# Performance work log

Measured on AMD Instinct MI355X. Metric: run time of the kernel, lower is better.

The kernel has to match this reference:

```python
import jax, jax.numpy as jnp
import numpy as np

B, C, H, W = 16, 512, 64, 64
SCALE = 8
CQK = C // SCALE  # 64
EPS = 1e-6


def setup_inputs() -> dict:
    key = jax.random.key(0)
    ks = jax.random.split(key, 8)
    x = jax.random.normal(ks[0], (B, C, H, W), dtype=jnp.float32)
    # 1x1 conv weights stored as [out_ch, in_ch] (kernel_size=1)
    Wq = jax.random.normal(ks[1], (CQK, C), dtype=jnp.float32) * 0.02
    bq = jnp.zeros((CQK,), dtype=jnp.float32)
    Wk = jax.random.normal(ks[2], (CQK, C), dtype=jnp.float32) * 0.02
    bk = jnp.zeros((CQK,), dtype=jnp.float32)
    Wv = jax.random.normal(ks[3], (C, C), dtype=jnp.float32) * 0.02
    bv = jnp.zeros((C,), dtype=jnp.float32)
    # gamma is initialized to 0 in the module; use a nonzero value so the
    # output is non-trivial for kernel correctness checks.
    gamma = jax.random.normal(ks[4], (1,), dtype=jnp.float32)
    return {"x": x, "Wq": Wq, "bq": bq, "Wk": Wk, "bk": bk,
            "Wv": Wv, "bv": bv, "gamma": gamma}


def _l2norm_ch(t):
    # normalize over the channel axis (dim=-2), matching torch.norm(p=2, dim=-2)
    nrm = jnp.sqrt(jnp.sum(t * t, axis=-2, keepdims=True))
    return t / jnp.maximum(nrm, EPS)


def reference(x, Wq, bq, Wk, bk, Wv, bv, gamma):
    b, c, h, w = x.shape
    n = h * w
    xf = x.reshape(b, c, n)                                   # [B,C,N]
    # 1x1 convs == channel matmuls
    Q = jnp.einsum('oc,bcn->bon', Wq, xf) + bq[None, :, None]  # [B,cqk,N]
    K = jnp.einsum('oc,bcn->bon', Wk, xf) + bk[None, :, None]  # [B,cqk,N]
    V = jnp.einsum('oc,bcn->bon', Wv, xf) + bv[None, :, None]  # [B,C,N]
    Qn = _l2norm_ch(Q).transpose(0, 2, 1)                      # [B,N,cqk]
    Kn = _l2norm_ch(K)                                         # [B,cqk,N]
    # Taylor-softmax surrogate denominator
    denom = n + jnp.einsum('bnc,bc->bn', Qn, Kn.sum(axis=-1))  # [B,N]
    tailor = 1.0 / jnp.maximum(denom, 1e-6)                    # [B,N]
    # KtV accumulation: [B,cqk,C]
    matrix = jnp.einsum('bmn,bcn->bmc', Kn, V)
    value_sum = jnp.sum(V, axis=-1)[:, :, None]                # [B,C,1] -> broadcast
    matrix_sum = value_sum + jnp.einsum('bnm,bmc->bcn', Qn, matrix)  # [B,C,N]
    weight_value = matrix_sum * tailor[:, None, :]             # [B,C,N]
    out = gamma * weight_value.reshape(b, c, h, w)
    return jnp.nan_to_num(out, nan=0.0, posinf=1.0, neginf=-1.0)
```

## Files before the change

### kernel.cpp

```cpp
#include <hip/hip_runtime.h>


typedef __attribute__((ext_vector_type(8))) short short8_t;
typedef __attribute__((ext_vector_type(4))) float f32x4;

__device__ __forceinline__ unsigned short f2bf(float f) {
  union { float f; unsigned u; } v; v.f = f;
  unsigned r = v.u + 0x7FFFu + ((v.u >> 16) & 1u);
  return (unsigned short)(r >> 16);
}
__device__ __forceinline__ float bf2f(unsigned short h) {
  union { unsigned u; float f; } v; v.u = ((unsigned)h) << 16;
  return v.f;
}

#define MFMA(a, b, c) __builtin_amdgcn_mfma_f32_16x16x32_bf16((a), (b), (c), 0, 0, 0)

__global__ void k_prep(const float* __restrict__ Wq, const float* __restrict__ Wk,
                       unsigned short* __restrict__ Wqk,
                       float* __restrict__ xsum, float* __restrict__ Ksum) {
  int idx = blockIdx.x * 256 + threadIdx.x;
  int o = idx >> 9, c = idx & 511;
  float v = (o < 64) ? Wq[o * 512 + c] : Wk[(o - 64) * 512 + c];
  Wqk[idx] = f2bf(v);
  if (idx < 8192) xsum[idx] = 0.f;
  if (idx < 1024) Ksum[idx] = 0.f;
}

__launch_bounds__(256, 2)
__global__ void k_qk(const float* __restrict__ x, const unsigned short* __restrict__ Wqk,
                     const float* __restrict__ bq, const float* __restrict__ bk,
                     unsigned short* __restrict__ QnT, unsigned short* __restrict__ KnG,
                     float* __restrict__ Ksum) {
  __shared__ __align__(16) unsigned char smem[77312];
  unsigned short* SAb[2] = {(unsigned short*)(smem + 0),
                            (unsigned short*)(smem + 18432)};
  unsigned short* SBb[2] = {(unsigned short*)(smem + 36864),
                            (unsigned short*)(smem + 55296)};
  unsigned short* EQ = (unsigned short*)(smem + 0);
  unsigned short* EK = (unsigned short*)(smem + 18432);
  float* ssq   = (float*)(smem + 73728);
  float* invq  = (float*)(smem + 75776);
  float* invk  = (float*)(smem + 76288);
  float* biasL = (float*)(smem + 76800);

  const int t = threadIdx.x;
  const int lane = t & 63, w = t >> 6;
  const int l15 = lane & 15, quad = lane >> 4;
  const int nt = blockIdx.x, b = blockIdx.y;
  const int n0 = nt * 128;
  const float* xb = x + (size_t)b * 512 * 4096;

  if (t < 128) biasL[t] = (t < 64) ? bq[t] : bk[t - 64];

  f32x4 acc[2][8];
#pragma unroll
  for (int i = 0; i < 2; ++i)
#pragma unroll
    for (int j = 0; j < 8; ++j) acc[i][j] = (f32x4){0.f, 0.f, 0.f, 0.f};

  const int nB = t & 127;
  const int cgB = t >> 7;
  const float* bsrc0 = xb + (size_t)(cgB * 32) * 4096 + n0 + nB;

  short8_t apre[4];
  float bpre[32];

#define QK_LOADA(kc_) do {                                                     \
    const int c0_ = (kc_) * 64;                                                \
    _Pragma("unroll")                                                          \
    for (int p = 0; p < 4; ++p) {                                              \
      int gid = t + p * 256; int o_ = gid >> 3, cg = gid & 7;                  \
      apre[p] = *(const short8_t*)(Wqk + o_ * 512 + c0_ + cg * 8);             \
    } } while (0)

#define QK_LOADB(kc_) do {                                                     \
    const float* s_ = bsrc0 + (size_t)(kc_) * 64 * 4096;                       \
    _Pragma("unroll")                                                          \
    for (int i = 0; i < 32; ++i) bpre[i] = s_[(size_t)i * 4096];               \
    } while (0)

#define QK_STORE(pb) do {                                                      \
    unsigned short* SAp = SAb[pb]; unsigned short* SBp = SBb[pb];              \
    _Pragma("unroll")                                                          \
    for (int p = 0; p < 4; ++p) {                                              \
      int gid = t + p * 256; int o_ = gid >> 3, cg = gid & 7;                  \
      *(short8_t*)(SAp + o_ * 72 + cg * 8) = apre[p];                          \
    }                                                                          \
    _Pragma("unroll")                                                          \
    for (int j = 0; j < 4; ++j) {                                              \
      short8_t v_;                                                             \
      _Pragma("unroll")                                                        \
      for (int e = 0; e < 8; ++e) v_[e] = (short)f2bf(bpre[j * 8 + e]);        \
      *(short8_t*)(SBp + nB * 72 + cgB * 32 + j * 8) = v_;                     \
    } } while (0)

#define QK_MM(pb) do {                                                         \
    const unsigned short* SAp = SAb[pb]; const unsigned short* SBp = SBb[pb];  \
    _Pragma("unroll")                                                          \
    for (int s = 0; s < 2; ++s) {                                              \
      short8_t a0 = *(const short8_t*)(SAp + (w * 32 + l15) * 72 + s * 32 + quad * 8);      \
      short8_t a1 = *(const short8_t*)(SAp + (w * 32 + 16 + l15) * 72 + s * 32 + quad * 8); \
      _Pragma("unroll")                                                        \
      for (int tc = 0; tc < 8; ++tc) {                                         \
        short8_t bf_ = *(const short8_t*)(SBp + (tc * 16 + l15) * 72 + s * 32 + quad * 8);  \
        acc[0][tc] = MFMA(a0, bf_, acc[0][tc]);                                \
        acc[1][tc] = MFMA(a1, bf_, acc[1][tc]);                                \
      } } } while (0)

  QK_LOADA(0); QK_LOADB(0);
#pragma unroll
  for (int kc = 0; kc < 8; ++kc) {
    const int pb = kc & 1;
    QK_STORE(pb);
    if (kc < 7) { QK_LOADA(kc + 1); QK_LOADB(kc + 1); }
    __syncthreads();
    QK_MM(pb);
  }
  __syncthreads();

#pragma unroll
  for (int trl = 0; trl < 2; ++trl)
#pragma unroll
    for (int reg = 0; reg < 4; ++reg) {
      int o = w * 32 + trl * 16 + quad * 4 + reg;
      float bias = biasL[o];
#pragma unroll
      for (int tc = 0; tc < 8; ++tc) acc[trl][tc][reg] += bias;
    }

#pragma unroll
  for (int tc = 0; tc < 8; ++tc) {
    float v = 0.f;
#pragma unroll
    for (int trl = 0; trl < 2; ++trl)
#pragma unroll
      for (int reg = 0; reg < 4; ++reg) {
        float q = acc[trl][tc][reg];
        v += q * q;
      }
    v += __shfl_xor(v, 16);
    v += __shfl_xor(v, 32);
    if (quad == 0) ssq[w * 128 + tc * 16 + l15] = v;
  }
  __syncthreads();
  if (t < 128) {
    float qs = ssq[t] + ssq[128 + t];
    float ks = ssq[256 + t] + ssq[384 + t];
    invq[t] = 1.0f / fmaxf(sqrtf(qs), 1e-6f);
    invk[t] = 1.0f / fmaxf(sqrtf(ks), 1e-6f);
  }
  __syncthreads();

  if (w < 2) {
#pragma unroll
    for (int trl = 0; trl < 2; ++trl)
#pragma unroll
      for (int tc = 0; tc < 8; ++tc) {
        int n = tc * 16 + l15;
        float inv = invq[n];
#pragma unroll
        for (int reg = 0; reg < 4; ++reg) {
          int o = w * 32 + trl * 16 + quad * 4 + reg;
          EQ[n * 72 + o] = f2bf(acc[trl][tc][reg] * inv);
        }
      }
  } else {
#pragma unroll
    for (int trl = 0; trl < 2; ++trl)
#pragma unroll
      for (int reg = 0; reg < 4; ++reg) {
        int m = (w - 2) * 32 + trl * 16 + quad * 4 + reg;
        float p = 0.f;
#pragma unroll
        for (int tc = 0; tc < 8; ++tc) {
          int n = tc * 16 + l15;
          float val = acc[trl][tc][reg] * invk[n];
          EK[m * 136 + n] = f2bf(val);
          p += val;
        }
        p += __shfl_xor(p, 1);
        p += __shfl_xor(p, 2);
        p += __shfl_xor(p, 4);
        p += __shfl_xor(p, 8);
        if (l15 == 0) atomicAdd(Ksum + b * 64 + m, p);
      }
  }
  __syncthreads();

  unsigned short* qdst = QnT + ((size_t)b * 4096 + n0) * 64;
#pragma unroll
  for (int p = 0; p < 4; ++p) {
    int idx = t + p * 256;
    int row = idx >> 3, seg = idx & 7;
    *(short8_t*)(qdst + row * 64 + seg * 8) = *(const short8_t*)(EQ + row * 72 + seg * 8);
  }
  unsigned short* kdst = KnG + (size_t)b * 64 * 4096 + n0;
#pragma unroll
  for (int p = 0; p < 4; ++p) {
    int idx = t + p * 256;
    int row = idx >> 4, seg = idx & 15;
    *(short8_t*)(kdst + (size_t)row * 4096 + seg * 8) =
        *(const short8_t*)(EK + row * 136 + seg * 8);
  }
#undef QK_LOADA
#undef QK_LOADB
#undef QK_STORE
#undef QK_MM
}

__launch_bounds__(256, 2)
__global__ void k_t(const float* __restrict__ x, const unsigned short* __restrict__ KnG,
                    float* __restrict__ Tpart, float* __restrict__ xsum,
                    const unsigned short* __restrict__ QnT,
                    const float* __restrict__ Ksum, float* __restrict__ tailor) {
  __shared__ __align__(16) unsigned char smem[55552];
  unsigned short* SAb[2] = {(unsigned short*)(smem + 0),
                            (unsigned short*)(smem + 9216)};
  unsigned short* SBb[2] = {(unsigned short*)(smem + 18432),
                            (unsigned short*)(smem + 36864)};
  float* Ksl = (float*)(smem + 55296);
  const int t = threadIdx.x;
  const int lane = t & 63, w = t >> 6;
  const int l15 = lane & 15, quad = lane >> 4;
  const int ns = blockIdx.x, ct = blockIdx.y, b = blockIdx.z;
  const int c0 = ct * 128;
  const float* xb = x + (size_t)b * 512 * 4096;
  const unsigned short* Knb = KnG + (size_t)b * 64 * 4096 + ns * 512;

  if (t < 64) Ksl[t] = Ksum[b * 64 + t];

  f32x4 acc[4][2];
#pragma unroll
  for (int i = 0; i < 4; ++i)
#pragma unroll
    for (int j = 0; j < 2; ++j) acc[i][j] = (f32x4){0.f, 0.f, 0.f, 0.f};

  const int row = t >> 1, half = t & 1;
  float xs = 0.f;
  const float* bbase = xb + (size_t)(c0 + row) * 4096 + ns * 512 + half * 32;

  short8_t apre[2];
  f32x4 bpre[8];

#define T_LOADA(ch_) do {                                                      \
    _Pragma("unroll")                                                          \
    for (int p = 0; p < 2; ++p) {                                              \
      int gid = t + p * 256; int m_ = gid >> 3, cg = gid & 7;                  \
      apre[p] = *(const short8_t*)(Knb + (size_t)m_ * 4096 + (ch_) * 64 + cg * 8); \
    } } while (0)

#define T_LOADB(ch_) do {                                                      \
    const float* s_ = bbase + (ch_) * 64;                                      \
    _Pragma("unroll")                                                          \
    for (int q = 0; q < 8; ++q) bpre[q] = *(const f32x4*)(s_ + q * 4);         \
    } while (0)

#define T_STORE(pb) do {                                                       \
    unsigned short* SAp = SAb[pb]; unsigned short* SBp = SBb[pb];              \
    _Pragma("unroll")                                                          \
    for (int p = 0; p < 2; ++p) {                                              \
      int gid = t + p * 256; int m_ = gid >> 3, cg = gid & 7;                  \
      *(short8_t*)(SAp + m_ * 72 + cg * 8) = apre[p];                          \
    }                                                                          \
    _Pragma("unroll")                                                          \
    for (int j = 0; j < 4; ++j) {                                              \
      short8_t v_;                                                             \
      _Pragma("unroll")                                                        \
      for (int e = 0; e < 4; ++e) {                                            \
        float f0 = bpre[j * 2][e], f1 = bpre[j * 2 + 1][e];                    \
        xs += f0 + f1;                                                         \
        v_[e] = (short)f2bf(f0); v_[4 + e] = (short)f2bf(f1);                  \
      }                                                                        \
      *(short8_t*)(SBp + row * 72 + half * 32 + j * 8) = v_;                   \
    } } while (0)

#define T_MM(pb) do {                                                          \
    const unsigned short* SAp = SAb[pb]; const unsigned short* SBp = SBb[pb];  \
    _Pragma("unroll")                                                          \
    for (int s = 0; s < 2; ++s) {                                              \
      short8_t af[4];                                                          \
      _Pragma("unroll")                                                        \
      for (int tm = 0; tm < 4; ++tm)                                           \
        af[tm] = *(const short8_t*)(SAp + (tm * 16 + l15) * 72 + s * 32 + quad * 8); \
      _Pragma("unroll")                                                        \
      for (int tcl = 0; tcl < 2; ++tcl) {                                      \
        short8_t bf_ = *(const short8_t*)(SBp + (w * 32 + tcl * 16 + l15) * 72 + s * 32 + quad * 8); \
        _Pragma("unroll")                                                      \
        for (int tm = 0; tm < 4; ++tm) acc[tm][tcl] = MFMA(af[tm], bf_, acc[tm][tcl]); \
      } } } while (0)

  T_LOADA(0); T_LOADB(0);
#pragma unroll
  for (int ch = 0; ch < 8; ++ch) {
    const int pb = ch & 1;
    T_STORE(pb);
    if (ch < 7) { T_LOADA(ch + 1); T_LOADB(ch + 1); }
    __syncthreads();
    if (ch == 0 && t < 128) {
      int n = ns * 512 + ct * 128 + t;
      const unsigned short* q = QnT + ((size_t)b * 4096 + n) * 64;
      float d = 0.f;
#pragma unroll
      for (int s8 = 0; s8 < 8; ++s8) {
        short8_t qv = *(const short8_t*)(q + s8 * 8);
#pragma unroll
        for (int e = 0; e < 8; ++e)
          d += bf2f((unsigned short)qv[e]) * Ksl[s8 * 8 + e];
      }
      tailor[b * 4096 + n] = 1.0f / fmaxf(4096.0f + d, 1e-6f);
    }
    T_MM(pb);
  }

  xs += __shfl_xor(xs, 1);
  if (half == 0) atomicAdd(xsum + b * 512 + c0 + row, xs);
  float* Tp = Tpart + ((size_t)(ns * 16 + b) * 64) * 512;
#pragma unroll
  for (int tm = 0; tm < 4; ++tm)
#pragma unroll
    for (int tcl = 0; tcl < 2; ++tcl)
#pragma unroll
      for (int reg = 0; reg < 4; ++reg) {
        int m = tm * 16 + quad * 4 + reg;
        int c = c0 + w * 32 + tcl * 16 + l15;
        Tp[(size_t)m * 512 + c] = acc[tm][tcl][reg];
      }
#undef T_LOADA
#undef T_LOADB
#undef T_STORE
#undef T_MM
}

__launch_bounds__(256, 2)
__global__ void k_mat(const float* __restrict__ Tpart, const float* __restrict__ Wv,
                      const float* __restrict__ bv, const float* __restrict__ xsum,
                      const float* __restrict__ Ksum,
                      unsigned short* __restrict__ matT, float* __restrict__ Vsum) {
  __shared__ __align__(16) unsigned char smem[27136];
  float* ST = (float*)smem;
  float* SW = (float*)(smem + 17408);
  float* SV = (float*)(smem + 26112);
  const int t = threadIdx.x;
  const int cb = blockIdx.x, b = blockIdx.y;
  const int c0 = cb * 32;
  const int mp = t >> 3, cs = t & 7;
  f32x4 acc0 = (f32x4){0.f, 0.f, 0.f, 0.f};
  f32x4 acc1 = (f32x4){0.f, 0.f, 0.f, 0.f};

  for (int kc = 0; kc < 8; ++kc) {
    __syncthreads();
#pragma unroll
    for (int p = 0; p < 4; ++p) {
      int idx = t + p * 256;
      int row = idx >> 4, f4 = idx & 15;
      const float* tp = Tpart + ((size_t)b * 64 + row) * 512 + kc * 64 + f4 * 4;
      f32x4 s = *(const f32x4*)tp;
#pragma unroll
      for (int ns2 = 1; ns2 < 8; ++ns2)
        s += *(const f32x4*)(tp + (size_t)ns2 * 524288);
      *(f32x4*)(ST + row * 68 + f4 * 4) = s;
    }
#pragma unroll
    for (int p = 0; p < 2; ++p) {
      int idx = t + p * 256;
      int row = idx >> 4, f4 = idx & 15;
      *(f32x4*)(SW + row * 68 + f4 * 4) =
          *(const f32x4*)(Wv + (size_t)(c0 + row) * 512 + kc * 64 + f4 * 4);
    }
    __syncthreads();
#pragma unroll 4
    for (int kk = 0; kk < 64; kk += 4) {
      f32x4 t0 = *(const f32x4*)(ST + (2 * mp) * 68 + kk);
      f32x4 t1 = *(const f32x4*)(ST + (2 * mp + 1) * 68 + kk);
#pragma unroll
      for (int j = 0; j < 4; ++j) {
        f32x4 wv = *(const f32x4*)(SW + (cs + j * 8) * 68 + kk);
#pragma unroll
        for (int e = 0; e < 4; ++e) {
          acc0[j] = fmaf(t0[e], wv[e], acc0[j]);
          acc1[j] = fmaf(t1[e], wv[e], acc1[j]);
        }
      }
    }
  }
  float ks0 = Ksum[b * 64 + 2 * mp];
  float ks1 = Ksum[b * 64 + 2 * mp + 1];
#pragma unroll
  for (int j = 0; j < 4; ++j) {
    int c = c0 + cs + j * 8;
    float bvc = bv[c];
    unsigned lo = f2bf(acc0[j] + bvc * ks0);
    unsigned hi = f2bf(acc1[j] + bvc * ks1);
    *(unsigned*)(matT + ((size_t)b * 512 + c) * 64 + 2 * mp) = lo | (hi << 16);
  }
  {
    int cc = t >> 3, kp = t & 7;
    const float* wr = Wv + (size_t)(c0 + cc) * 512 + kp * 64;
    const float* xr = xsum + b * 512 + kp * 64;
    float s = 0.f;
    for (int i = 0; i < 64; ++i) s += wr[i] * xr[i];
    SV[cc * 8 + kp] = s;
  }
  __syncthreads();
  if (t < 32) {
    float s = 0.f;
#pragma unroll
    for (int i = 0; i < 8; ++i) s += SV[t * 8 + i];
    int c = c0 + t;
    Vsum[b * 512 + c] = s + 4096.0f * bv[c];
  }
}

__launch_bounds__(256, 2)
__global__ void k_out(const unsigned short* __restrict__ QnT,
                      const unsigned short* __restrict__ matT,
                      const float* __restrict__ tailG, const float* __restrict__ Vsum,
                      const float* __restrict__ gamma, float* __restrict__ out) {
  __shared__ __align__(16) unsigned char smem[37888];
  unsigned short* SA = (unsigned short*)smem;
  unsigned short* SB = (unsigned short*)(smem + 18432);
  float* tail = (float*)(smem + 36864);
  float* vs   = (float*)(smem + 37376);
  const int t = threadIdx.x;
  const int lane = t & 63, w = t >> 6;
  const int l15 = lane & 15, quad = lane >> 4;
  const int nt = blockIdx.x, ct = blockIdx.y, b = blockIdx.z;
  const int n0 = nt * 128, c0 = ct * 128;

  const unsigned short* asrc = matT + ((size_t)b * 512 + c0) * 64;
  const unsigned short* bsrc = QnT + ((size_t)b * 4096 + n0) * 64;
#pragma unroll
  for (int p = 0; p < 4; ++p) {
    int idx = t + p * 256;
    int row = idx >> 3, seg = idx & 7;
    *(short8_t*)(SA + row * 72 + seg * 8) = *(const short8_t*)(asrc + row * 64 + seg * 8);
    *(short8_t*)(SB + row * 72 + seg * 8) = *(const short8_t*)(bsrc + row * 64 + seg * 8);
  }
  if (t < 128) tail[t] = tailG[b * 4096 + n0 + t];
  else if (t < 256) vs[t - 128] = Vsum[b * 512 + c0 + (t - 128)];
  __syncthreads();

  f32x4 acc[2][8];
#pragma unroll
  for (int i = 0; i < 2; ++i)
#pragma unroll
    for (int j = 0; j < 8; ++j) acc[i][j] = (f32x4){0.f, 0.f, 0.f, 0.f};

#pragma unroll
  for (int s = 0; s < 2; ++s) {
    short8_t a0 = *(const short8_t*)(SA + (w * 32 + l15) * 72 + s * 32 + quad * 8);
    short8_t a1 = *(const short8_t*)(SA + (w * 32 + 16 + l15) * 72 + s * 32 + quad * 8);
#pragma unroll
    for (int tc = 0; tc < 8; ++tc) {
      short8_t bfr = *(const short8_t*)(SB + (tc * 16 + l15) * 72 + s * 32 + quad * 8);
      acc[0][tc] = MFMA(a0, bfr, acc[0][tc]);
      acc[1][tc] = MFMA(a1, bfr, acc[1][tc]);
    }
  }
  const float g = gamma[0];
  float* ob = out + (size_t)b * 512 * 4096;
#pragma unroll
  for (int trl = 0; trl < 2; ++trl)
#pragma unroll
    for (int tc = 0; tc < 8; ++tc) {
      int n = tc * 16 + l15;
      float tl = tail[n] * g;
#pragma unroll
      for (int reg = 0; reg < 4; ++reg) {
        int cl = w * 32 + trl * 16 + quad * 4 + reg;
        float val = tl * (vs[cl] + acc[trl][tc][reg]);
        ob[(size_t)(c0 + cl) * 4096 + n0 + n] = val;
      }
    }
}

extern "C" void kernel_launch(void* const* d_in, const int* in_sizes, int n_in,
                              void* d_out, int out_size, void* d_ws, size_t ws_size,
                              hipStream_t stream) {
  const float* x     = (const float*)d_in[0];
  const float* Wq    = (const float*)d_in[1];
  const float* bq    = (const float*)d_in[2];
  const float* Wk    = (const float*)d_in[3];
  const float* bk    = (const float*)d_in[4];
  const float* Wv    = (const float*)d_in[5];
  const float* bv    = (const float*)d_in[6];
  const float* gamma = (const float*)d_in[7];
  float* out = (float*)d_out;
  char* ws = (char*)d_ws;

  float* Tpart  = (float*)(ws + 0);
  float* xsum   = (float*)(ws + 16777216);
  float* Ksum   = (float*)(ws + 16809984);
  float* Vsum   = (float*)(ws + 16814080);
  float* tailor = (float*)(ws + 16846848);
  unsigned short* Wqk  = (unsigned short*)(ws + 17108992);
  unsigned short* matT = (unsigned short*)(ws + 17240064);
  unsigned short* QnT  = (unsigned short*)(ws + 18288640);
  unsigned short* Kn   = (unsigned short*)(ws + 26677248);

  k_prep<<<256, 256, 0, stream>>>(Wq, Wk, Wqk, xsum, Ksum);
  k_qk<<<dim3(32, 16), 256, 0, stream>>>(x, Wqk, bq, bk, QnT, Kn, Ksum);
  k_t<<<dim3(8, 4, 16), 256, 0, stream>>>(x, Kn, Tpart, xsum, QnT, Ksum, tailor);
  k_mat<<<dim3(16, 16), 256, 0, stream>>>(Tpart, Wv, bv, xsum, Ksum, matT, Vsum);
  k_out<<<dim3(32, 4, 16), 256, 0, stream>>>(QnT, matT, tailor, Vsum, gamma, out);
}
```

Baseline: 324.9 us.

## Split Tpart reduction into separate kernel and loop k_out over channel tiles

Adds a k_red kernel that sums the 8 split-N partials of T once, so k_mat no longer re-reads all 8 partial slabs in every one of its 16 channel blocks. k_out now runs one block per (n-tile, batch) and loops over the 4 channel tiles. It reuses the staged QnT tile from shared memory and double-buffers matT tiles, prefetching the next tile into registers. The costs are an extra launch, an extra T buffer round-trip, and 4x fewer k_out blocks with larger shared memory, which lowers parallelism.

```diff
diff --git a/kernel.cpp b/kernel.cpp
--- a/kernel.cpp
+++ b/kernel.cpp
@@ -332,8 +332,17 @@
 #undef T_MM
 }
 
+__global__ void k_red(const float* __restrict__ Tpart, float* __restrict__ T) {
+  size_t idx = (size_t)blockIdx.x * 256 + threadIdx.x;
+  const f32x4* p = (const f32x4*)Tpart + idx;
+  f32x4 s = p[0];
+#pragma unroll
+  for (int ns = 1; ns < 8; ++ns) s += p[(size_t)ns * 131072];
+  ((f32x4*)T)[idx] = s;
+}
+
 __launch_bounds__(256, 2)
-__global__ void k_mat(const float* __restrict__ Tpart, const float* __restrict__ Wv,
+__global__ void k_mat(const float* __restrict__ T, const float* __restrict__ Wv,
                       const float* __restrict__ bv, const float* __restrict__ xsum,
                       const float* __restrict__ Ksum,
                       unsigned short* __restrict__ matT, float* __restrict__ Vsum) {
@@ -354,12 +363,8 @@
     for (int p = 0; p < 4; ++p) {
       int idx = t + p * 256;
       int row = idx >> 4, f4 = idx & 15;
-      const float* tp = Tpart + ((size_t)b * 64 + row) * 512 + kc * 64 + f4 * 4;
-      f32x4 s = *(const f32x4*)tp;
-#pragma unroll
-      for (int ns2 = 1; ns2 < 8; ++ns2)
-        s += *(const f32x4*)(tp + (size_t)ns2 * 524288);
-      *(f32x4*)(ST + row * 68 + f4 * 4) = s;
+      *(f32x4*)(ST + row * 68 + f4 * 4) =
+          *(const f32x4*)(T + ((size_t)b * 64 + row) * 512 + kc * 64 + f4 * 4);
     }
 #pragma unroll
     for (int p = 0; p < 2; ++p) {
@@ -417,62 +422,87 @@
                       const unsigned short* __restrict__ matT,
                       const float* __restrict__ tailG, const float* __restrict__ Vsum,
                       const float* __restrict__ gamma, float* __restrict__ out) {
-  __shared__ __align__(16) unsigned char smem[37888];
-  unsigned short* SA = (unsigned short*)smem;
-  unsigned short* SB = (unsigned short*)(smem + 18432);
-  float* tail = (float*)(smem + 36864);
-  float* vs   = (float*)(smem + 37376);
+  __shared__ __align__(16) unsigned char smem[57856];
+  unsigned short* SB = (unsigned short*)(smem + 36864);
+  float* tail = (float*)(smem + 55296);
+  float* vs   = (float*)(smem + 55808);
   const int t = threadIdx.x;
   const int lane = t & 63, w = t >> 6;
   const int l15 = lane & 15, quad = lane >> 4;
-  const int nt = blockIdx.x, ct = blockIdx.y, b = blockIdx.z;
-  const int n0 = nt * 128, c0 = ct * 128;
-
-  const unsigned short* asrc = matT + ((size_t)b * 512 + c0) * 64;
+  const int nt = blockIdx.x, b = blockIdx.y;
+  const int n0 = nt * 128;
+
   const unsigned short* bsrc = QnT + ((size_t)b * 4096 + n0) * 64;
 #pragma unroll
   for (int p = 0; p < 4; ++p) {
     int idx = t + p * 256;
     int row = idx >> 3, seg = idx & 7;
-    *(short8_t*)(SA + row * 72 + seg * 8) = *(const short8_t*)(asrc + row * 64 + seg * 8);
     *(short8_t*)(SB + row * 72 + seg * 8) = *(const short8_t*)(bsrc + row * 64 + seg * 8);
   }
   if (t < 128) tail[t] = tailG[b * 4096 + n0 + t];
-  else if (t < 256) vs[t - 128] = Vsum[b * 512 + c0 + (t - 128)];
-  __syncthreads();
-
-  f32x4 acc[2][8];
-#pragma unroll
-  for (int i = 0; i < 2; ++i)
-#pragma unroll
-    for (int j = 0; j < 8; ++j) acc[i][j] = (f32x4){0.f, 0.f, 0.f, 0.f};
-
-#pragma unroll
-  for (int s = 0; s < 2; ++s) {
-    short8_t a0 = *(const short8_t*)(SA + (w * 32 + l15) * 72 + s * 32 + quad * 8);
-    short8_t a1 = *(const short8_t*)(SA + (w * 32 + 16 + l15) * 72 + s * 32 + quad * 8);
-#pragma unroll
-    for (int tc = 0; tc < 8; ++tc) {
-      short8_t bfr = *(const short8_t*)(SB + (tc * 16 + l15) * 72 + s * 32 + quad * 8);
-      acc[0][tc] = MFMA(a0, bfr, acc[0][tc]);
-      acc[1][tc] = MFMA(a1, bfr, acc[1][tc]);
-    }
-  }
+  vs[t] = Vsum[b * 512 + t];
+  vs[256 + t] = Vsum[b * 512 + 256 + t];
   const float g = gamma[0];
   float* ob = out + (size_t)b * 512 * 4096;
-#pragma unroll
-  for (int trl = 0; trl < 2; ++trl)
-#pragma unroll
-    for (int tc = 0; tc < 8; ++tc) {
-      int n = tc * 16 + l15;
-      float tl = tail[n] * g;
-#pragma unroll
-      for (int reg = 0; reg < 4; ++reg) {
-        int cl = w * 32 + trl * 16 + quad * 4 + reg;
-        float val = tl * (vs[cl] + acc[trl][tc][reg]);
-        ob[(size_t)(c0 + cl) * 4096 + n0 + n] = val;
-      }
-    }
+  const unsigned short* asrc = matT + (size_t)b * 512 * 64;
+
+  short8_t areg[4];
+#pragma unroll
+  for (int p = 0; p < 4; ++p) {
+    int idx = t + p * 256;
+    int row = idx >> 3, seg = idx & 7;
+    areg[p] = *(const short8_t*)(asrc + row * 64 + seg * 8);
+  }
+  for (int ct = 0; ct < 4; ++ct) {
+    unsigned short* SAp = (unsigned short*)(smem + (ct & 1) * 18432);
+#pragma unroll
+    for (int p = 0; p < 4; ++p) {
+      int idx = t + p * 256;
+      int row = idx >> 3, seg = idx & 7;
+      *(short8_t*)(SAp + row * 72 + seg * 8) = areg[p];
+    }
+    if (ct < 3) {
+      const unsigned short* an = asrc + (size_t)(ct + 1) * 128 * 64;
+#pragma unroll
+      for (int p = 0; p < 4; ++p) {
+        int idx = t + p * 256;
+        int row = idx >> 3, seg = idx & 7;
+        areg[p] = *(const short8_t*)(an + row * 64 + seg * 8);
+      }
+    }
+    __syncthreads();
+    f32x4 acc[2][8];
+#pragma unroll
+    for (int i = 0; i < 2; ++i)
+#pragma unroll
+      for (int j = 0; j < 8; ++j) acc[i][j] = (f32x4){0.f, 0.f, 0.f, 0.f};
+#pragma unroll
+    for (int s = 0; s < 2; ++s) {
+      short8_t a0 = *(const short8_t*)(SAp + (w * 32 + l15) * 72 + s * 32 + quad * 8);
+      short8_t a1 = *(const short8_t*)(SAp + (w * 32 + 16 + l15) * 72 + s * 32 + quad * 8);
+#pragma unroll
+      for (int tc = 0; tc < 8; ++tc) {
+        short8_t bfr = *(const short8_t*)(SB + (tc * 16 + l15) * 72 + s * 32 + quad * 8);
+        acc[0][tc] = MFMA(a0, bfr, acc[0][tc]);
+        acc[1][tc] = MFMA(a1, bfr, acc[1][tc]);
+      }
+    }
+    const int c0 = ct * 128;
+#pragma unroll
+    for (int trl = 0; trl < 2; ++trl)
+#pragma unroll
+      for (int tc = 0; tc < 8; ++tc) {
+        int n = tc * 16 + l15;
+        float tl = tail[n] * g;
+#pragma unroll
+        for (int reg = 0; reg < 4; ++reg) {
+          int cl = w * 32 + trl * 16 + quad * 4 + reg;
+          float val = tl * (vs[c0 + cl] + acc[trl][tc][reg]);
+          ob[(size_t)(c0 + cl) * 4096 + n0 + n] = val;
+        }
+      }
+    __syncthreads();
+  }
 }
 
 extern "C" void kernel_launch(void* const* d_in, const int* in_sizes, int n_in,
@@ -490,18 +520,20 @@
   char* ws = (char*)d_ws;
 
   float* Tpart  = (float*)(ws + 0);
-  float* xsum   = (float*)(ws + 16777216);
-  float* Ksum   = (float*)(ws + 16809984);
-  float* Vsum   = (float*)(ws + 16814080);
-  float* tailor = (float*)(ws + 16846848);
-  unsigned short* Wqk  = (unsigned short*)(ws + 17108992);
-  unsigned short* matT = (unsigned short*)(ws + 17240064);
-  unsigned short* QnT  = (unsigned short*)(ws + 18288640);
-  unsigned short* Kn   = (unsigned short*)(ws + 26677248);
+  float* T      = (float*)(ws + 16777216);
+  float* xsum   = (float*)(ws + 18874368);
+  float* Ksum   = (float*)(ws + 18907136);
+  float* Vsum   = (float*)(ws + 18911232);
+  float* tailor = (float*)(ws + 18944000);
+  unsigned short* Wqk  = (unsigned short*)(ws + 19206144);
+  unsigned short* matT = (unsigned short*)(ws + 19337216);
+  unsigned short* QnT  = (unsigned short*)(ws + 20385792);
+  unsigned short* Kn   = (unsigned short*)(ws + 28774400);
 
   k_prep<<<256, 256, 0, stream>>>(Wq, Wk, Wqk, xsum, Ksum);
   k_qk<<<dim3(32, 16), 256, 0, stream>>>(x, Wqk, bq, bk, QnT, Kn, Ksum);
   k_t<<<dim3(8, 4, 16), 256, 0, stream>>>(x, Kn, Tpart, xsum, QnT, Ksum, tailor);
-  k_mat<<<dim3(16, 16), 256, 0, stream>>>(Tpart, Wv, bv, xsum, Ksum, matT, Vsum);
-  k_out<<<dim3(32, 4, 16), 256, 0, stream>>>(QnT, matT, tailor, Vsum, gamma, out);
-}
+  k_red<<<512, 256, 0, stream>>>(Tpart, T);
+  k_mat<<<dim3(16, 16), 256, 0, stream>>>(T, Wv, bv, xsum, Ksum, matT, Vsum);
+  k_out<<<dim3(32, 16), 256, 0, stream>>>(QnT, matT, tailor, Vsum, gamma, out);
+}
```

New measurement: 320.9 us (median of 2 runs). About the same (-1.2%).
